# Kernel tuning notes

Measured on AMD Instinct MI355X. Metric: run time of the kernel, lower is better.

## Reference

```python
import jax, jax.numpy as jnp
import numpy as np

LN_EPS = 1e-5

def setup_inputs() -> dict:
    key = jax.random.key(0)
    ks = jax.random.split(key, 12)
    B, S, M, C, D = 16, 1024, 4096, 768, 256
    inp = {
        'seed_xyz_norm': jax.random.normal(ks[0], (B, S, 3), jnp.float32),
        'p_last': jax.random.normal(ks[1], (B, M, 3), jnp.float32),
        'f_last': jax.random.normal(ks[2], (B, C, M), jnp.float32),
        'seed_features': jax.random.normal(ks[3], (B, D, S), jnp.float32),
        # LayerNorm params over C
        'ln_gamma': jnp.ones((C,), jnp.float32),
        'ln_beta': jnp.zeros((C,), jnp.float32),
        # conv1d projector C -> 256 (kernel size 1) + ReLU
        'proj_w': jax.random.normal(ks[4], (D, C), jnp.float32) * (1.0 / np.sqrt(C)),
        'proj_b': jnp.zeros((D,), jnp.float32),
        # fusion MLP: concat512 -> 512 -> 256 (1x1 convs)
        'mlp_w1': jax.random.normal(ks[5], (2 * D, 2 * D), jnp.float32) * (1.0 / np.sqrt(2 * D)),
        'mlp_b1': jnp.zeros((2 * D,), jnp.float32),
        'mlp_w2': jax.random.normal(ks[6], (D, 2 * D), jnp.float32) * (1.0 / np.sqrt(2 * D)),
        'mlp_b2': jnp.zeros((D,), jnp.float32),
    }
    return inp


def reference(seed_xyz_norm, p_last, f_last, seed_features,
              ln_gamma, ln_beta, proj_w, proj_b,
              mlp_w1, mlp_b1, mlp_w2, mlp_b2):
    # --- nearest_neighbor_gather_features ---
    # squared distance [B,S,M]; argmin over M, gather features [B,C,S]
    d2 = jnp.sum(seed_xyz_norm * seed_xyz_norm, -1, keepdims=True) \
         - 2.0 * jnp.einsum('bsd,bmd->bsm', seed_xyz_norm, p_last) \
         + jnp.sum(p_last * p_last, -1)[:, None, :]
    idx = jnp.argmin(d2, axis=-1)                                   # [B,S]
    lift3d_raw = jnp.take_along_axis(f_last, idx[:, None, :], axis=2)  # [B,C,S]

    # --- LayerNorm over channel dim C ---
    mu = jnp.mean(lift3d_raw, axis=1, keepdims=True)
    var = jnp.mean((lift3d_raw - mu) ** 2, axis=1, keepdims=True)
    x_ln = (lift3d_raw - mu) * jax.lax.rsqrt(var + LN_EPS)
    x_ln = x_ln * ln_gamma[None, :, None] + ln_beta[None, :, None]

    # --- conv1d projector (1x1) + ReLU ---
    proj = jax.nn.relu(jnp.einsum('oc,bcs->bos', proj_w, x_ln) + proj_b[None, :, None])

    # --- concat fusion MLP ---
    fused = jnp.concatenate([seed_features, proj], axis=1)          # [B,512,S]
    h = jax.nn.relu(jnp.einsum('oc,bcs->bos', mlp_w1, fused) + mlp_b1[None, :, None])
    mixed = jnp.einsum('oc,bcs->bos', mlp_w2, h) + mlp_b2[None, :, None]  # [B,256,S]
    return mixed
```

## Files before the change

### kernel.cpp

```cpp
#include <hip/hip_runtime.h>

namespace {

constexpr int B = 16, S = 1024, M = 4096, C = 768, D = 256;
constexpr int N = B * S;

typedef __attribute__((ext_vector_type(8))) short bf16x8;
typedef __attribute__((ext_vector_type(4))) float f32x4;

__device__ inline ushort f2bf(float f) {
  uint u = __float_as_uint(f);
  uint r = (u + 0x7FFFu + ((u >> 16) & 1u)) >> 16;
  return (ushort)r;
}

__device__ __forceinline__ void g2lds16(const ushort* g, ushort* l) {
  __builtin_amdgcn_global_load_lds(
      (const __attribute__((address_space(1))) uint*)g,
      (__attribute__((address_space(3))) uint*)l, 16, 0, 0);
}

__global__ __launch_bounds__(256)
void nn_kernel(const float* __restrict__ xyz, const float* __restrict__ p,
               int* __restrict__ idx_out) {
  const int b = blockIdx.y;
  const int t = threadIdx.x;
  const int seed = blockIdx.x * 16 + (t >> 4);
  const int l16 = t & 15;

  const float sx = xyz[((size_t)b * S + seed) * 3 + 0];
  const float sy = xyz[((size_t)b * S + seed) * 3 + 1];
  const float sz = xyz[((size_t)b * S + seed) * 3 + 2];
  const float ss = __fadd_rn(__fadd_rn(__fmul_rn(sx, sx), __fmul_rn(sy, sy)),
                             __fmul_rn(sz, sz));

  __shared__ float4 pt[256];

  float best = 3.4028235e38f;
  int besti = 0;
  const float* pb = p + (size_t)b * M * 3;

  for (int m0 = 0; m0 < M; m0 += 256) {
    __syncthreads();
    {
      const float a0 = pb[(size_t)(m0 + t) * 3 + 0];
      const float a1 = pb[(size_t)(m0 + t) * 3 + 1];
      const float a2 = pb[(size_t)(m0 + t) * 3 + 2];
      const float pp = __fadd_rn(__fadd_rn(__fmul_rn(a0, a0), __fmul_rn(a1, a1)),
                                 __fmul_rn(a2, a2));
      pt[t] = make_float4(a0, a1, a2, pp);
    }
    __syncthreads();
    #pragma unroll 4
    for (int j = l16; j < 256; j += 16) {
      const float4 q = pt[j];
      float dot = __fmul_rn(sx, q.x);
      dot = __fadd_rn(dot, __fmul_rn(sy, q.y));
      dot = __fadd_rn(dot, __fmul_rn(sz, q.z));
      const float d2 = __fadd_rn(__fsub_rn(ss, __fmul_rn(2.0f, dot)), q.w);
      const int mi = m0 + j;
      if (d2 < best || (d2 == best && mi < besti)) { best = d2; besti = mi; }
    }
  }
  #pragma unroll
  for (int off = 8; off >= 1; off >>= 1) {
    const float ob = __shfl_xor(best, off, 16);
    const int   oi = __shfl_xor(besti, off, 16);
    if (ob < best || (ob == best && oi < besti)) { best = ob; besti = oi; }
  }
  if (l16 == 0) idx_out[b * S + seed] = besti;
}

__global__ __launch_bounds__(512)
void sort_kernel(const int* __restrict__ idx, int* __restrict__ sIdx,
                 int* __restrict__ sS) {
  const int b = blockIdx.x;
  const int t = threadIdx.x;
  __shared__ int key[1024];
  __shared__ int val[1024];
  key[t] = idx[b * S + t];             val[t] = t;
  key[t + 512] = idx[b * S + t + 512]; val[t + 512] = t + 512;
  __syncthreads();
  for (int k = 2; k <= 1024; k <<= 1) {
    for (int j = k >> 1; j > 0; j >>= 1) {
      #pragma unroll 2
      for (int i = t; i < 1024; i += 512) {
        const int p = i ^ j;
        if (p > i) {
          const bool up = ((i & k) == 0);
          const int ki = key[i], kp = key[p];
          if ((ki > kp) == up) {
            key[i] = kp; key[p] = ki;
            const int tv = val[i]; val[i] = val[p]; val[p] = tv;
          }
        }
      }
      __syncthreads();
    }
  }
  sIdx[b * S + t] = key[t];             sS[b * S + t] = val[t];
  sIdx[b * S + t + 512] = key[t + 512]; sS[b * S + t + 512] = val[t + 512];
}

__global__ __launch_bounds__(256)
void gatherT_kernel(const float* __restrict__ f, const int* __restrict__ sIdx,
                    const int* __restrict__ sS, float* __restrict__ tmp) {
  const int b = blockIdx.y;
  const int m0 = blockIdx.x * 64;
  const int t = threadIdx.x;
  __shared__ float tile[64][65];
  __shared__ int bound[2];

  if (t < 2) {
    const int target = m0 + (t ? 64 : 0);
    int lo = 0, hi = S;
    while (lo < hi) {
      const int mid = (lo + hi) >> 1;
      if (sIdx[b * S + mid] < target) lo = mid + 1; else hi = mid;
    }
    bound[t] = lo;
  }
  __syncthreads();
  const int lo = bound[0];
  const int cnt = bound[1] - bound[0];
  if (cnt == 0) return;

  const float* fb = f + (size_t)b * C * M + m0;
  const int wv = t >> 6;
  const int ml = t & 63;

  for (int cc = 0; cc < 12; ++cc) {
    __syncthreads();
    const int c0 = cc * 64;
    #pragma unroll
    for (int q = 0; q < 16; ++q) {
      const int cl = q * 4 + wv;
      tile[cl][ml] = fb[(size_t)(c0 + cl) * M + ml];
    }
    __syncthreads();
    for (int i0 = 0; i0 < cnt; i0 += 4) {
      const int i = i0 + wv;
      if (i < cnt) {
        const int r = lo + i;
        const int mloc = sIdx[b * S + r] - m0;
        const int s = sS[b * S + r];
        tmp[((size_t)b * S + s) * C + c0 + ml] = tile[ml][mloc];
      }
    }
  }
}

__global__ __launch_bounds__(256)
void ln_kernel(const float* __restrict__ tmp,
               const float* __restrict__ gamma, const float* __restrict__ beta,
               ushort* __restrict__ xln) {
  const int n = blockIdx.y * 1024 + blockIdx.x;
  const int t = threadIdx.x;
  const float* row = tmp + (size_t)n * C;
  const float v0 = row[t], v1 = row[t + 256], v2 = row[t + 512];

  __shared__ float red[4];
  __shared__ float stats[2];
  const int wave = t >> 6;

  float ps = v0 + v1 + v2;
  #pragma unroll
  for (int off = 32; off >= 1; off >>= 1) ps += __shfl_xor(ps, off);
  if ((t & 63) == 0) red[wave] = ps;
  __syncthreads();
  if (t == 0) stats[0] = (red[0] + red[1] + red[2] + red[3]) * (1.0f / 768.0f);
  __syncthreads();
  const float mu = stats[0];

  const float d0 = v0 - mu, d1 = v1 - mu, d2 = v2 - mu;
  float pv = d0 * d0 + d1 * d1 + d2 * d2;
  #pragma unroll
  for (int off = 32; off >= 1; off >>= 1) pv += __shfl_xor(pv, off);
  if ((t & 63) == 0) red[wave] = pv;
  __syncthreads();
  if (t == 0) {
    const float var = (red[0] + red[1] + red[2] + red[3]) * (1.0f / 768.0f);
    stats[1] = 1.0f / sqrtf(var + 1e-5f);
  }
  __syncthreads();
  const float rs = stats[1];

  ushort* ob = xln + (size_t)n * C;
  ob[t      ] = f2bf((d0 * rs) * gamma[t      ] + beta[t      ]);
  ob[t + 256] = f2bf((d1 * rs) * gamma[t + 256] + beta[t + 256]);
  ob[t + 512] = f2bf((d2 * rs) * gamma[t + 512] + beta[t + 512]);
}

__global__ __launch_bounds__(256)
void transpose_sf_kernel(const float* __restrict__ sf, ushort* __restrict__ fused) {
  const int b = blockIdx.z;
  const int d0 = blockIdx.y * 64;
  const int s0 = blockIdx.x * 64;
  const int t = threadIdx.x;
  __shared__ float tile[64][68];

  const float* inb = sf + ((size_t)b * D + d0) * S + s0;
  #pragma unroll
  for (int q = 0; q < 4; ++q) {
    const int rr = (t >> 4) + q * 16;
    const int c4 = (t & 15) * 4;
    const float4 v = *(const float4*)&inb[(size_t)rr * S + c4];
    *(float4*)&tile[rr][c4] = v;
  }
  __syncthreads();
  #pragma unroll
  for (int q = 0; q < 4; ++q) {
    const int srow = (t >> 4) + q * 16;
    const int dc = (t & 15) * 4;
    ushort4 o;
    o.x = f2bf(tile[dc + 0][srow]);
    o.y = f2bf(tile[dc + 1][srow]);
    o.z = f2bf(tile[dc + 2][srow]);
    o.w = f2bf(tile[dc + 3][srow]);
    *(ushort4*)&fused[((size_t)b * S + s0 + srow) * 512 + d0 + dc] = o;
  }
}

__global__ __launch_bounds__(256)
void convert_w_kernel(const float* __restrict__ w0, int n0, ushort* __restrict__ o0,
                      const float* __restrict__ w1, int n1, ushort* __restrict__ o1,
                      const float* __restrict__ w2, int n2, ushort* __restrict__ o2) {
  const int which = blockIdx.y;
  const float* src = which == 0 ? w0 : which == 1 ? w1 : w2;
  ushort* dst = which == 0 ? o0 : which == 1 ? o1 : o2;
  const int n = which == 0 ? n0 : which == 1 ? n1 : n2;
  const int i = (blockIdx.x * 256 + threadIdx.x) * 4;
  if (i < n) {
    const float4 v = *(const float4*)&src[i];
    ushort4 o;
    o.x = f2bf(v.x); o.y = f2bf(v.y); o.z = f2bf(v.z); o.w = f2bf(v.w);
    *(ushort4*)&dst[i] = o;
  }
}

__global__ __launch_bounds__(256, 2)
void gemm_bf16_kernel(const ushort* __restrict__ W, int K, int O,
                      const ushort* __restrict__ X,
                      const float* __restrict__ bias,
                      void* __restrict__ out, int outMode, int ldOut, int colOff,
                      int relu) {
  const int n0 = blockIdx.x * 64;
  const int o0 = blockIdx.y * 128;
  const int t = threadIdx.x;
  const int w = t >> 6;
  const int lane = t & 63;
  const int l16 = lane & 15;
  const int quad = lane >> 4;
  const int wo = w >> 1;
  const int wsd = w & 1;

  __shared__ ushort Wt[128 * 32];
  __shared__ ushort Xt[64 * 32];
  __shared__ float biasS[128];
  if (t < 128) biasS[t] = bias[o0 + t];

  f32x4 acc[4][2];
  const f32x4 z = {0.f, 0.f, 0.f, 0.f};
  #pragma unroll
  for (int of = 0; of < 4; ++of) { acc[of][0] = z; acc[of][1] = z; }

  const int srow = lane >> 2;
  const int chk = lane & 3;

  for (int c0 = 0; c0 < K; c0 += 32) {
    __syncthreads();
    #pragma unroll
    for (int q = 0; q < 2; ++q) {
      const int r = w * 32 + q * 16 + srow;
      const int cc = chk ^ (r & 3);
      g2lds16(&W[(size_t)(o0 + r) * K + c0 + cc * 8], &Wt[(w * 32 + q * 16) * 32]);
    }
    {
      const int r = w * 16 + srow;
      const int cc = chk ^ (r & 3);
      g2lds16(&X[(size_t)(n0 + r) * K + c0 + cc * 8], &Xt[(w * 16) * 32]);
    }
    __syncthreads();

    bf16x8 bfr[2];
    #pragma unroll
    for (int sf = 0; sf < 2; ++sf) {
      const int sr = wsd * 32 + sf * 16 + l16;
      bfr[sf] = *(const bf16x8*)&Xt[sr * 32 + ((quad ^ (sr & 3)) * 8)];
    }
    #pragma unroll
    for (int of = 0; of < 4; ++of) {
      const int orr = wo * 64 + of * 16 + l16;
      const bf16x8 afr = *(const bf16x8*)&Wt[orr * 32 + ((quad ^ (orr & 3)) * 8)];
      acc[of][0] = __builtin_amdgcn_mfma_f32_16x16x32_bf16(afr, bfr[0], acc[of][0], 0, 0, 0);
      acc[of][1] = __builtin_amdgcn_mfma_f32_16x16x32_bf16(afr, bfr[1], acc[of][1], 0, 0, 0);
    }
  }

  if (outMode == 0) {
    ushort* ob = (ushort*)out;
    #pragma unroll
    for (int of = 0; of < 4; ++of) {
      #pragma unroll
      for (int sf = 0; sf < 2; ++sf) {
        const int n = n0 + wsd * 32 + sf * 16 + l16;
        const int ol = wo * 64 + of * 16 + quad * 4;
        float v0 = acc[of][sf].x + biasS[ol + 0];
        float v1 = acc[of][sf].y + biasS[ol + 1];
        float v2 = acc[of][sf].z + biasS[ol + 2];
        float v3 = acc[of][sf].w + biasS[ol + 3];
        if (relu) {
          v0 = fmaxf(v0, 0.f); v1 = fmaxf(v1, 0.f);
          v2 = fmaxf(v2, 0.f); v3 = fmaxf(v3, 0.f);
        }
        ushort4 st;
        st.x = f2bf(v0); st.y = f2bf(v1); st.z = f2bf(v2); st.w = f2bf(v3);
        *(ushort4*)&ob[(size_t)n * ldOut + colOff + o0 + ol] = st;
      }
    }
  } else {
    float* o32 = (float*)out;
    #pragma unroll
    for (int of = 0; of < 4; ++of) {
      #pragma unroll
      for (int sf = 0; sf < 2; ++sf) {
        const int n = n0 + wsd * 32 + sf * 16 + l16;
        const int ol = wo * 64 + of * 16 + quad * 4;
        const int bb = n >> 10, s = n & 1023;
        const float vr[4] = {acc[of][sf].x, acc[of][sf].y, acc[of][sf].z, acc[of][sf].w};
        #pragma unroll
        for (int r = 0; r < 4; ++r) {
          const int o = o0 + ol + r;
          o32[((size_t)bb * O + o) * S + s] = vr[r] + biasS[ol + r];
        }
      }
    }
  }
}

}

extern "C" void kernel_launch(void* const* d_in, const int* in_sizes, int n_in,
                              void* d_out, int out_size, void* d_ws, size_t ws_size,
                              hipStream_t stream) {
  const float* seed_xyz  = (const float*)d_in[0];
  const float* p_last    = (const float*)d_in[1];
  const float* f_last    = (const float*)d_in[2];
  const float* seed_feat = (const float*)d_in[3];
  const float* ln_gamma  = (const float*)d_in[4];
  const float* ln_beta   = (const float*)d_in[5];
  const float* proj_w    = (const float*)d_in[6];
  const float* proj_b    = (const float*)d_in[7];
  const float* mlp_w1    = (const float*)d_in[8];
  const float* mlp_b1    = (const float*)d_in[9];
  const float* mlp_w2    = (const float*)d_in[10];
  const float* mlp_b2    = (const float*)d_in[11];
  float* out = (float*)d_out;

  char* ws = (char*)d_ws;
  int*    idx   = (int*)(ws);
  int*    sIdx  = (int*)(ws + (64 << 10));
  int*    sS    = (int*)(ws + (128 << 10));
  ushort* wp_bf = (ushort*)(ws + (256 << 10));
  ushort* w1_bf = (ushort*)(ws + (640 << 10));
  ushort* w2_bf = (ushort*)(ws + (1152 << 10));
  float*  tmp   = (float*)(ws + (2ull << 20));
  ushort* xln   = (ushort*)(ws + (50ull << 20));
  ushort* fused = (ushort*)(ws + (74ull << 20));
  ushort* hbuf  = (ushort*)(ws + (90ull << 20));

  nn_kernel<<<dim3(S / 16, B), 256, 0, stream>>>(seed_xyz, p_last, idx);
  sort_kernel<<<dim3(B), 512, 0, stream>>>(idx, sIdx, sS);

  gatherT_kernel<<<dim3(M / 64, B), 256, 0, stream>>>(f_last, sIdx, sS, tmp);
  ln_kernel<<<dim3(1024, B), 256, 0, stream>>>(tmp, ln_gamma, ln_beta, xln);

  transpose_sf_kernel<<<dim3(S / 64, D / 64, B), 256, 0, stream>>>(seed_feat, fused);
  convert_w_kernel<<<dim3(256, 3), 256, 0, stream>>>(
      proj_w, D * C, wp_bf, mlp_w1, 512 * 512, w1_bf, mlp_w2, 256 * 512, w2_bf);

  gemm_bf16_kernel<<<dim3(N / 64, 256 / 128), 256, 0, stream>>>(
      wp_bf, C, 256, xln, proj_b, fused, 0, 512, 256, 1);

  gemm_bf16_kernel<<<dim3(N / 64, 512 / 128), 256, 0, stream>>>(
      w1_bf, 512, 512, fused, mlp_b1, hbuf, 0, 512, 0, 1);

  gemm_bf16_kernel<<<dim3(N / 64, 256 / 128), 256, 0, stream>>>(
      w2_bf, 512, 256, hbuf, mlp_b2, out, 1, 0, 0, 0);
}
```

Measured before the change: 457.5 us.

## Fuse projector and MLP GEMMs into one kernel keeping intermediates in LDS

The three separate bf16 GEMM launches are replaced by one kernel. Each block handles 32 tokens and computes the projector, the first MLP layer in two halves, and the second layer, holding the proj and hidden activations in swizzled LDS instead of writing them to global memory. The gathered-feature scratch buffer also drops from fp32 to bf16 before LayerNorm, halving that traffic but adding a rounding step before normalization. Every block now re-streams all weight matrices through LDS with only 32 tokens of reuse, and the large LDS footprint limits occupancy.

```diff
diff --git a/kernel.cpp b/kernel.cpp
--- a/kernel.cpp
+++ b/kernel.cpp
@@ -13,11 +13,26 @@
   uint r = (u + 0x7FFFu + ((u >> 16) & 1u)) >> 16;
   return (ushort)r;
 }
+__device__ inline float bf2f(ushort u) {
+  return __uint_as_float(((uint)u) << 16);
+}
 
 __device__ __forceinline__ void g2lds16(const ushort* g, ushort* l) {
   __builtin_amdgcn_global_load_lds(
       (const __attribute__((address_space(1))) uint*)g,
       (__attribute__((address_space(3))) uint*)l, 16, 0, 0);
+}
+
+__device__ __forceinline__ void stage16(const ushort* __restrict__ src, int ldk,
+                                        int r0, int c0, ushort* dst, int lane) {
+  const int sr = lane >> 2, ck = lane & 3;
+  const int r = r0 + sr;
+  const int cc = ck ^ (r & 3);
+  g2lds16(&src[(size_t)r * ldk + c0 + cc * 8], dst + r0 * 32);
+}
+
+__device__ __forceinline__ int swz32(int row, int ch) {
+  return row * 256 + (ch ^ (row & 7)) * 8;
 }
 
 __global__ __launch_bounds__(256)
@@ -104,7 +119,7 @@
 
 __global__ __launch_bounds__(256)
 void gatherT_kernel(const float* __restrict__ f, const int* __restrict__ sIdx,
-                    const int* __restrict__ sS, float* __restrict__ tmp) {
+                    const int* __restrict__ sS, ushort* __restrict__ tmp) {
   const int b = blockIdx.y;
   const int m0 = blockIdx.x * 64;
   const int t = threadIdx.x;
@@ -144,20 +159,20 @@
         const int r = lo + i;
         const int mloc = sIdx[b * S + r] - m0;
         const int s = sS[b * S + r];
-        tmp[((size_t)b * S + s) * C + c0 + ml] = tile[ml][mloc];
-      }
-    }
-  }
-}
-
-__global__ __launch_bounds__(256)
-void ln_kernel(const float* __restrict__ tmp,
+        tmp[((size_t)b * S + s) * C + c0 + ml] = f2bf(tile[ml][mloc]);
+      }
+    }
+  }
+}
+
+__global__ __launch_bounds__(256)
+void ln_kernel(const ushort* __restrict__ tmp,
                const float* __restrict__ gamma, const float* __restrict__ beta,
                ushort* __restrict__ xln) {
   const int n = blockIdx.y * 1024 + blockIdx.x;
   const int t = threadIdx.x;
-  const float* row = tmp + (size_t)n * C;
-  const float v0 = row[t], v1 = row[t + 256], v2 = row[t + 512];
+  const ushort* row = tmp + (size_t)n * C;
+  const float v0 = bf2f(row[t]), v1 = bf2f(row[t + 256]), v2 = bf2f(row[t + 512]);
 
   __shared__ float red[4];
   __shared__ float stats[2];
@@ -192,7 +207,7 @@
 }
 
 __global__ __launch_bounds__(256)
-void transpose_sf_kernel(const float* __restrict__ sf, ushort* __restrict__ fused) {
+void transpose_sf_kernel(const float* __restrict__ sf, ushort* __restrict__ seedT) {
   const int b = blockIdx.z;
   const int d0 = blockIdx.y * 64;
   const int s0 = blockIdx.x * 64;
@@ -217,7 +232,7 @@
     o.y = f2bf(tile[dc + 1][srow]);
     o.z = f2bf(tile[dc + 2][srow]);
     o.w = f2bf(tile[dc + 3][srow]);
-    *(ushort4*)&fused[((size_t)b * S + s0 + srow) * 512 + d0 + dc] = o;
+    *(ushort4*)&seedT[((size_t)b * S + s0 + srow) * 256 + d0 + dc] = o;
   }
 }
 
@@ -238,102 +253,173 @@
   }
 }
 
-__global__ __launch_bounds__(256, 2)
-void gemm_bf16_kernel(const ushort* __restrict__ W, int K, int O,
-                      const ushort* __restrict__ X,
-                      const float* __restrict__ bias,
-                      void* __restrict__ out, int outMode, int ldOut, int colOff,
-                      int relu) {
-  const int n0 = blockIdx.x * 64;
-  const int o0 = blockIdx.y * 128;
+__global__ __launch_bounds__(256)
+void fused_mlp_kernel(const ushort* __restrict__ xln,
+                      const ushort* __restrict__ seedT,
+                      const ushort* __restrict__ wp, const ushort* __restrict__ w1,
+                      const ushort* __restrict__ w2,
+                      const float* __restrict__ pb, const float* __restrict__ b1,
+                      const float* __restrict__ b2, float* __restrict__ out) {
+  const int n0 = blockIdx.x * 32;
   const int t = threadIdx.x;
   const int w = t >> 6;
   const int lane = t & 63;
   const int l16 = lane & 15;
   const int quad = lane >> 4;
-  const int wo = w >> 1;
-  const int wsd = w & 1;
-
-  __shared__ ushort Wt[128 * 32];
-  __shared__ ushort Xt[64 * 32];
-  __shared__ float biasS[128];
-  if (t < 128) biasS[t] = bias[o0 + t];
-
-  f32x4 acc[4][2];
+
+  __shared__ ushort Wt[256 * 32];
+  __shared__ ushort Xt[32 * 32];
+  __shared__ ushort projL[32 * 256];
+  __shared__ ushort hL[32 * 256];
+  __shared__ float biasS[1024];
+
+  biasS[t] = pb[t];
+  biasS[256 + t] = b1[t];
+  biasS[512 + t] = b1[256 + t];
+  biasS[768 + t] = b2[t];
+
   const f32x4 z = {0.f, 0.f, 0.f, 0.f};
-  #pragma unroll
-  for (int of = 0; of < 4; ++of) { acc[of][0] = z; acc[of][1] = z; }
-
-  const int srow = lane >> 2;
-  const int chk = lane & 3;
-
-  for (int c0 = 0; c0 < K; c0 += 32) {
-    __syncthreads();
-    #pragma unroll
-    for (int q = 0; q < 2; ++q) {
-      const int r = w * 32 + q * 16 + srow;
-      const int cc = chk ^ (r & 3);
-      g2lds16(&W[(size_t)(o0 + r) * K + c0 + cc * 8], &Wt[(w * 32 + q * 16) * 32]);
-    }
-    {
-      const int r = w * 16 + srow;
-      const int cc = chk ^ (r & 3);
-      g2lds16(&X[(size_t)(n0 + r) * K + c0 + cc * 8], &Xt[(w * 16) * 32]);
-    }
-    __syncthreads();
-
-    bf16x8 bfr[2];
+
+  {
+    f32x4 accP[4][2];
+    #pragma unroll
+    for (int of = 0; of < 4; ++of) { accP[of][0] = z; accP[of][1] = z; }
+
+    const ushort* xb = xln + (size_t)n0 * C;
+    for (int c0 = 0; c0 < C; c0 += 32) {
+      __syncthreads();
+      #pragma unroll
+      for (int q = 0; q < 4; ++q) stage16(wp, C, w * 64 + q * 16, c0, Wt, lane);
+      if (w < 2) stage16(xb, C, w * 16, c0, Xt, lane);
+      __syncthreads();
+
+      bf16x8 bx[2];
+      #pragma unroll
+      for (int sf = 0; sf < 2; ++sf) {
+        const int sr = sf * 16 + l16;
+        bx[sf] = *(const bf16x8*)&Xt[sr * 32 + ((quad ^ (sr & 3)) * 8)];
+      }
+      #pragma unroll
+      for (int of = 0; of < 4; ++of) {
+        const int orr = w * 64 + of * 16 + l16;
+        const bf16x8 afr = *(const bf16x8*)&Wt[orr * 32 + ((quad ^ (orr & 3)) * 8)];
+        accP[of][0] = __builtin_amdgcn_mfma_f32_16x16x32_bf16(afr, bx[0], accP[of][0], 0, 0, 0);
+        accP[of][1] = __builtin_amdgcn_mfma_f32_16x16x32_bf16(afr, bx[1], accP[of][1], 0, 0, 0);
+      }
+    }
+    __syncthreads();
+    #pragma unroll
+    for (int of = 0; of < 4; ++of) {
+      #pragma unroll
+      for (int sf = 0; sf < 2; ++sf) {
+        const int s = sf * 16 + l16;
+        const int o = w * 64 + of * 16 + quad * 4;
+        ushort4 st;
+        st.x = f2bf(fmaxf(accP[of][sf].x + biasS[o + 0], 0.f));
+        st.y = f2bf(fmaxf(accP[of][sf].y + biasS[o + 1], 0.f));
+        st.z = f2bf(fmaxf(accP[of][sf].z + biasS[o + 2], 0.f));
+        st.w = f2bf(fmaxf(accP[of][sf].w + biasS[o + 3], 0.f));
+        *(ushort4*)&projL[swz32(s, o >> 3) + (o & 7)] = st;
+      }
+    }
+  }
+
+  f32x4 accO[4][2];
+  #pragma unroll
+  for (int of = 0; of < 4; ++of) { accO[of][0] = z; accO[of][1] = z; }
+
+  const ushort* stb = seedT + (size_t)n0 * 256;
+
+  for (int hh = 0; hh < 2; ++hh) {
+    f32x4 accH[4][2];
+    #pragma unroll
+    for (int of = 0; of < 4; ++of) { accH[of][0] = z; accH[of][1] = z; }
+
+    const ushort* w1h = w1 + (size_t)(hh * 256) * 512;
+    for (int c0 = 0; c0 < 512; c0 += 32) {
+      __syncthreads();
+      #pragma unroll
+      for (int q = 0; q < 4; ++q) stage16(w1h, 512, w * 64 + q * 16, c0, Wt, lane);
+      if (c0 < 256 && w < 2) stage16(stb, 256, w * 16, c0, Xt, lane);
+      __syncthreads();
+
+      bf16x8 bx[2];
+      if (c0 < 256) {
+        #pragma unroll
+        for (int sf = 0; sf < 2; ++sf) {
+          const int sr = sf * 16 + l16;
+          bx[sf] = *(const bf16x8*)&Xt[sr * 32 + ((quad ^ (sr & 3)) * 8)];
+        }
+      } else {
+        #pragma unroll
+        for (int sf = 0; sf < 2; ++sf) {
+          const int sr = sf * 16 + l16;
+          bx[sf] = *(const bf16x8*)&projL[swz32(sr, ((c0 - 256) >> 3) + quad)];
+        }
+      }
+      #pragma unroll
+      for (int of = 0; of < 4; ++of) {
+        const int orr = w * 64 + of * 16 + l16;
+        const bf16x8 afr = *(const bf16x8*)&Wt[orr * 32 + ((quad ^ (orr & 3)) * 8)];
+        accH[of][0] = __builtin_amdgcn_mfma_f32_16x16x32_bf16(afr, bx[0], accH[of][0], 0, 0, 0);
+        accH[of][1] = __builtin_amdgcn_mfma_f32_16x16x32_bf16(afr, bx[1], accH[of][1], 0, 0, 0);
+      }
+    }
+    __syncthreads();
+    #pragma unroll
+    for (int of = 0; of < 4; ++of) {
+      #pragma unroll
+      for (int sf = 0; sf < 2; ++sf) {
+        const int s = sf * 16 + l16;
+        const int o = w * 64 + of * 16 + quad * 4;
+        const float bb0 = biasS[256 + hh * 256 + o];
+        ushort4 st;
+        st.x = f2bf(fmaxf(accH[of][sf].x + biasS[256 + hh * 256 + o + 0], 0.f));
+        st.y = f2bf(fmaxf(accH[of][sf].y + biasS[256 + hh * 256 + o + 1], 0.f));
+        st.z = f2bf(fmaxf(accH[of][sf].z + biasS[256 + hh * 256 + o + 2], 0.f));
+        st.w = f2bf(fmaxf(accH[of][sf].w + biasS[256 + hh * 256 + o + 3], 0.f));
+        (void)bb0;
+        *(ushort4*)&hL[swz32(s, o >> 3) + (o & 7)] = st;
+      }
+    }
+
+    for (int c0 = 0; c0 < 256; c0 += 32) {
+      __syncthreads();
+      #pragma unroll
+      for (int q = 0; q < 4; ++q)
+        stage16(w2 + hh * 256, 512, w * 64 + q * 16, c0, Wt, lane);
+      __syncthreads();
+
+      bf16x8 bx[2];
+      #pragma unroll
+      for (int sf = 0; sf < 2; ++sf) {
+        const int sr = sf * 16 + l16;
+        bx[sf] = *(const bf16x8*)&hL[swz32(sr, (c0 >> 3) + quad)];
+      }
+      #pragma unroll
+      for (int of = 0; of < 4; ++of) {
+        const int orr = w * 64 + of * 16 + l16;
+        const bf16x8 afr = *(const bf16x8*)&Wt[orr * 32 + ((quad ^ (orr & 3)) * 8)];
+        accO[of][0] = __builtin_amdgcn_mfma_f32_16x16x32_bf16(afr, bx[0], accO[of][0], 0, 0, 0);
+        accO[of][1] = __builtin_amdgcn_mfma_f32_16x16x32_bf16(afr, bx[1], accO[of][1], 0, 0, 0);
+      }
+    }
+    __syncthreads();
+  }
+
+  const int b = n0 >> 10;
+  const int sbase = n0 & 1023;
+  #pragma unroll
+  for (int of = 0; of < 4; ++of) {
     #pragma unroll
     for (int sf = 0; sf < 2; ++sf) {
-      const int sr = wsd * 32 + sf * 16 + l16;
-      bfr[sf] = *(const bf16x8*)&Xt[sr * 32 + ((quad ^ (sr & 3)) * 8)];
-    }
-    #pragma unroll
-    for (int of = 0; of < 4; ++of) {
-      const int orr = wo * 64 + of * 16 + l16;
-      const bf16x8 afr = *(const bf16x8*)&Wt[orr * 32 + ((quad ^ (orr & 3)) * 8)];
-      acc[of][0] = __builtin_amdgcn_mfma_f32_16x16x32_bf16(afr, bfr[0], acc[of][0], 0, 0, 0);
-      acc[of][1] = __builtin_amdgcn_mfma_f32_16x16x32_bf16(afr, bfr[1], acc[of][1], 0, 0, 0);
-    }
-  }
-
-  if (outMode == 0) {
-    ushort* ob = (ushort*)out;
-    #pragma unroll
-    for (int of = 0; of < 4; ++of) {
-      #pragma unroll
-      for (int sf = 0; sf < 2; ++sf) {
-        const int n = n0 + wsd * 32 + sf * 16 + l16;
-        const int ol = wo * 64 + of * 16 + quad * 4;
-        float v0 = acc[of][sf].x + biasS[ol + 0];
-        float v1 = acc[of][sf].y + biasS[ol + 1];
-        float v2 = acc[of][sf].z + biasS[ol + 2];
-        float v3 = acc[of][sf].w + biasS[ol + 3];
-        if (relu) {
-          v0 = fmaxf(v0, 0.f); v1 = fmaxf(v1, 0.f);
-          v2 = fmaxf(v2, 0.f); v3 = fmaxf(v3, 0.f);
-        }
-        ushort4 st;
-        st.x = f2bf(v0); st.y = f2bf(v1); st.z = f2bf(v2); st.w = f2bf(v3);
-        *(ushort4*)&ob[(size_t)n * ldOut + colOff + o0 + ol] = st;
-      }
-    }
-  } else {
-    float* o32 = (float*)out;
-    #pragma unroll
-    for (int of = 0; of < 4; ++of) {
-      #pragma unroll
-      for (int sf = 0; sf < 2; ++sf) {
-        const int n = n0 + wsd * 32 + sf * 16 + l16;
-        const int ol = wo * 64 + of * 16 + quad * 4;
-        const int bb = n >> 10, s = n & 1023;
-        const float vr[4] = {acc[of][sf].x, acc[of][sf].y, acc[of][sf].z, acc[of][sf].w};
-        #pragma unroll
-        for (int r = 0; r < 4; ++r) {
-          const int o = o0 + ol + r;
-          o32[((size_t)bb * O + o) * S + s] = vr[r] + biasS[ol + r];
-        }
-      }
+      const int s = sbase + sf * 16 + l16;
+      const int o = w * 64 + of * 16 + quad * 4;
+      const float vr[4] = {accO[of][sf].x, accO[of][sf].y,
+                           accO[of][sf].z, accO[of][sf].w};
+      #pragma unroll
+      for (int r = 0; r < 4; ++r)
+        out[((size_t)b * 256 + o + r) * S + s] = vr[r] + biasS[768 + o + r];
     }
   }
 }
@@ -364,10 +450,9 @@
   ushort* wp_bf = (ushort*)(ws + (256 << 10));
   ushort* w1_bf = (ushort*)(ws + (640 << 10));
   ushort* w2_bf = (ushort*)(ws + (1152 << 10));
-  float*  tmp   = (float*)(ws + (2ull << 20));
-  ushort* xln   = (ushort*)(ws + (50ull << 20));
-  ushort* fused = (ushort*)(ws + (74ull << 20));
-  ushort* hbuf  = (ushort*)(ws + (90ull << 20));
+  ushort* tmp   = (ushort*)(ws + (2ull << 20));
+  ushort* xln   = (ushort*)(ws + (26ull << 20));
+  ushort* seedT = (ushort*)(ws + (50ull << 20));
 
   nn_kernel<<<dim3(S / 16, B), 256, 0, stream>>>(seed_xyz, p_last, idx);
   sort_kernel<<<dim3(B), 512, 0, stream>>>(idx, sIdx, sS);
@@ -375,16 +460,10 @@
   gatherT_kernel<<<dim3(M / 64, B), 256, 0, stream>>>(f_last, sIdx, sS, tmp);
   ln_kernel<<<dim3(1024, B), 256, 0, stream>>>(tmp, ln_gamma, ln_beta, xln);
 
-  transpose_sf_kernel<<<dim3(S / 64, D / 64, B), 256, 0, stream>>>(seed_feat, fused);
+  transpose_sf_kernel<<<dim3(S / 64, D / 64, B), 256, 0, stream>>>(seed_feat, seedT);
   convert_w_kernel<<<dim3(256, 3), 256, 0, stream>>>(
       proj_w, D * C, wp_bf, mlp_w1, 512 * 512, w1_bf, mlp_w2, 256 * 512, w2_bf);
 
-  gemm_bf16_kernel<<<dim3(N / 64, 256 / 128), 256, 0, stream>>>(
-      wp_bf, C, 256, xln, proj_b, fused, 0, 512, 256, 1);
-
-  gemm_bf16_kernel<<<dim3(N / 64, 512 / 128), 256, 0, stream>>>(
-      w1_bf, 512, 512, fused, mlp_b1, hbuf, 0, 512, 0, 1);
-
-  gemm_bf16_kernel<<<dim3(N / 64, 256 / 128), 256, 0, stream>>>(
-      w2_bf, 512, 256, hbuf, mlp_b2, out, 1, 0, 0, 0);
-}
+  fused_mlp_kernel<<<dim3(N / 32), 256, 0, stream>>>(
+      xln, seedT, wp_bf, w1_bf, w2_bf, proj_b, mlp_b1, mlp_b2, out);
+}
```

After: 450.2 us. No clear change (-1.6%).
